# Kernel optimization log

Hardware: AMD Instinct MI355X
Metric: run time of the kernel (lower is better)

Reference implementation:

```python
import jax, jax.numpy as jnp
import numpy as np

B, V, C, G, D, H, W, N = 1, 4, 32, 8, 8, 240, 320, 9
EPS = 1e-5  # BatchNorm3d default eps


def grid_sample(img, grid, align_corners, zeros_pad):
    # img [B,C,Hs,Ws], grid [B,Hg,Wg,2] normalized coords; mirrors torch F.grid_sample bilinear
    Bi, Ci, Hs, Ws = img.shape
    gx, gy = grid[..., 0], grid[..., 1]
    if align_corners:
        ix = (gx + 1.0) * 0.5 * (Ws - 1)
        iy = (gy + 1.0) * 0.5 * (Hs - 1)
    else:
        ix = ((gx + 1.0) * Ws - 1.0) * 0.5
        iy = ((gy + 1.0) * Hs - 1.0) * 0.5
    x0 = jnp.floor(ix)
    y0 = jnp.floor(iy)
    wx1 = ix - x0
    wy1 = iy - y0

    def corner(xi, yi, wgt):
        xc = jnp.clip(xi, 0, Ws - 1).astype(jnp.int32)
        yc = jnp.clip(yi, 0, Hs - 1).astype(jnp.int32)
        v = jax.vmap(lambda im, yy, xx: im[:, yy, xx])(img, yc, xc)  # [B,C,Hg,Wg]
        if zeros_pad:
            valid = ((xi >= 0) & (xi <= Ws - 1) & (yi >= 0) & (yi <= Hs - 1)).astype(img.dtype)
            wgt = wgt * valid
        return v * wgt[:, None]

    return (corner(x0, y0, (1 - wx1) * (1 - wy1)) + corner(x0 + 1, y0, wx1 * (1 - wy1))
            + corner(x0, y0 + 1, (1 - wx1) * wy1) + corner(x0 + 1, y0 + 1, wx1 * wy1))


def differentiable_warping(src_fea, src_proj, ref_proj, depth):
    # src_fea [B,Cf,H,W], projs [B,4,4], depth [B,D,H,W] -> [B,Cf,D,H,W]
    Bi, Cf, Hs, Ws = src_fea.shape
    Dd = depth.shape[1]
    proj = src_proj @ jnp.linalg.inv(ref_proj)
    rot, trans = proj[:, :3, :3], proj[:, :3, 3:4]
    yy, xx = jnp.meshgrid(jnp.arange(Hs, dtype=jnp.float32), jnp.arange(Ws, dtype=jnp.float32), indexing='ij')
    xyz = jnp.stack([xx.ravel(), yy.ravel(), jnp.ones(Hs * Ws, jnp.float32)], axis=0)  # [3,HW]
    rot_xyz = jnp.einsum('bij,jk->bik', rot, xyz)  # [B,3,HW]
    pxyz = rot_xyz[:, :, None, :] * depth.reshape(Bi, 1, Dd, Hs * Ws) + trans[:, :, :, None]  # [B,3,D,HW]
    neg = pxyz[:, 2] <= 1e-3
    px = jnp.where(neg, float(Ws), pxyz[:, 0])
    py = jnp.where(neg, float(Hs), pxyz[:, 1])
    pz = jnp.where(neg, 1.0, pxyz[:, 2])
    gx = (px / pz) / ((Ws - 1) / 2.0) - 1.0
    gy = (py / pz) / ((Hs - 1) / 2.0) - 1.0
    grid = jnp.stack([gx, gy], axis=-1).reshape(Bi, Dd * Hs, Ws, 2)
    grid = jax.lax.stop_gradient(grid)  # torch builds the warp grid under no_grad
    warped = grid_sample(src_fea, grid, align_corners=True, zeros_pad=True)  # [B,Cf,D*H,W]
    return warped.reshape(Bi, Cf, Dd, Hs, Ws)


def conv_bn_relu(x, w, bn):
    # 1x1x1 Conv3d (no bias) + BatchNorm3d (inference) + ReLU; x [B,Ci,D,H,W]
    y = jnp.einsum('oi,bidhw->bodhw', w, x)
    g, b, m, v = bn
    s = g / jnp.sqrt(v + EPS)
    return jax.nn.relu(y * s[:, None, None, None] + (b - m * s)[:, None, None, None])


def conv1(x, w, b):
    return jnp.einsum('oi,bidhw->bodhw', w, x) + b[:, None, None, None]


def pixel_wise_net(sim, w0, bn0, w1, bn1, w2, b2):
    y = conv_bn_relu(sim, w0, bn0)
    y = conv_bn_relu(y, w1, bn1)
    y = jax.nn.sigmoid(conv1(y, w2, b2))[:, 0]  # [B,D,H,W]
    return jnp.max(y, axis=1, keepdims=True)  # [B,1,H,W]


def _forward(ref_feature, src_features, ref_proj, src_projs, depth_sample, grid, weight,
             pw_w0, pw_bn0, pw_w1, pw_bn1, pw_w2, pw_b2,
             sn_w0, sn_bn0, sn_w1, sn_bn1, sn_w2, sn_b2):
    Bi, Cf, Hs, Ws = ref_feature.shape
    Gq = pw_w0.shape[1]
    Dd = depth_sample.shape[1]
    ref_g = ref_feature.reshape(Bi, Gq, Cf // Gq, 1, Hs, Ws)
    sim_sum = jnp.zeros((Bi, Gq, Dd, Hs, Ws), jnp.float32)
    w_sum = jnp.zeros((Bi, 1, 1, Hs, Ws), jnp.float32)
    vws = []
    for v in range(src_features.shape[0]):  # small fixed view count
        warped = differentiable_warping(src_features[v], src_projs[v], ref_proj, depth_sample)
        warped = warped.reshape(Bi, Gq, Cf // Gq, Dd, Hs, Ws)
        sim = jnp.mean(warped * ref_g, axis=2)  # [B,G,D,H,W] group correlation
        vw = pixel_wise_net(sim, pw_w0, pw_bn0, pw_w1, pw_bn1, pw_w2, pw_b2)  # [B,1,H,W]
        vws.append(vw)
        sim_sum = sim_sum + sim * vw[:, :, None]
        w_sum = w_sum + vw[:, :, None]
    x = sim_sum / w_sum
    # SimilarityNet: conv stack -> neighbor grid_sample -> adaptive weighted sum
    y = conv_bn_relu(x, sn_w0, sn_bn0)
    y = conv_bn_relu(y, sn_w1, sn_bn1)
    y = conv1(y, sn_w2, sn_b2)[:, 0]  # [B,D,H,W]
    s = grid_sample(y, grid, align_corners=False, zeros_pad=False)  # border pad, [B,D,N*H,W]
    Nn = grid.shape[1] // Hs
    s = s.reshape(Bi, Dd, Nn, Hs, Ws)
    score_vol = jnp.sum(s * weight, axis=2)  # [B,D,H,W]
    score = jax.nn.softmax(score_vol, axis=1)  # exp(log_softmax) == softmax
    depth = jnp.sum(depth_sample * score, axis=1)  # [B,H,W] (is_inverse=False)
    view_weights = jax.lax.stop_gradient(jnp.concatenate(vws, axis=1))  # [B,V,H,W]
    return depth, score, view_weights


def setup_inputs():
    key = jax.random.key(0)
    ks = jax.random.split(key, 20)
    ref_feature = jax.random.normal(ks[0], (B, C, H, W), jnp.float32)
    src_features = jax.random.normal(ks[1], (V, B, C, H, W), jnp.float32)
    f = 500.0
    K = np.array([[f, 0, W / 2.0, 0], [0, f, H / 2.0, 0], [0, 0, 1, 0], [0, 0, 0, 1]], np.float32)
    ref_proj = jnp.asarray(np.tile(K[None], (B, 1, 1)))
    sp = []
    for tx, ty in [(20.0, 0.0), (-20.0, 0.0), (0.0, 10.0), (0.0, -10.0)]:
        E = np.eye(4, dtype=np.float32)
        E[0, 3], E[1, 3] = tx, ty
        sp.append(np.tile((K @ E)[None], (B, 1, 1)))
    src_projs = jnp.asarray(np.stack(sp))
    depth_sample = jnp.sort(425.0 + 510.0 * jax.random.uniform(ks[2], (B, D, H, W), jnp.float32), axis=1)
    # evaluation neighbor grid: per-pixel +-3px learned-style offsets, align_corners=False normalization
    dx = jax.random.uniform(ks[3], (B, N, H, W), minval=-3.0, maxval=3.0)
    dy = jax.random.uniform(ks[4], (B, N, H, W), minval=-3.0, maxval=3.0)
    xs = jnp.arange(W, dtype=jnp.float32)[None, None, None, :]
    ys = jnp.arange(H, dtype=jnp.float32)[None, None, :, None]
    gx = (2.0 * (xs + dx) + 1.0) / W - 1.0
    gy = (2.0 * (ys + dy) + 1.0) / H - 1.0
    grid = jnp.stack([gx, gy], -1).reshape(B, N * H, W, 2)
    weight = jax.random.uniform(ks[5], (B, D, N, H, W), jnp.float32)  # feature*depth weight in (0,1)

    def bn(k, c):
        k1, k2, k3, k4 = jax.random.split(k, 4)
        return jnp.stack([1.0 + 0.1 * jax.random.normal(k1, (c,)), 0.1 * jax.random.normal(k2, (c,)),
                          0.01 * jax.random.normal(k3, (c,)), 1.0 + 0.1 * jax.random.uniform(k4, (c,))])

    return dict(ref_feature=ref_feature, src_features=src_features, ref_proj=ref_proj,
                src_projs=src_projs, depth_sample=depth_sample, grid=grid, weight=weight,
                pw_w0=0.1 * jax.random.normal(ks[6], (16, G)), pw_bn0=bn(ks[7], 16),
                pw_w1=0.1 * jax.random.normal(ks[8], (8, 16)), pw_bn1=bn(ks[9], 8),
                pw_w2=0.1 * jax.random.normal(ks[10], (1, 8)), pw_b2=jnp.zeros((1,), jnp.float32),
                sn_w0=0.1 * jax.random.normal(ks[11], (16, G)), sn_bn0=bn(ks[12], 16),
                sn_w1=0.1 * jax.random.normal(ks[13], (8, 16)), sn_bn1=bn(ks[14], 8),
                sn_w2=0.1 * jax.random.normal(ks[15], (1, 8)), sn_b2=jnp.zeros((1,), jnp.float32))


def reference(ref_feature, src_features, ref_proj, src_projs, depth_sample, grid, weight,
              pw_w0, pw_bn0, pw_w1, pw_bn1, pw_w2, pw_b2,
              sn_w0, sn_bn0, sn_w1, sn_bn1, sn_w2, sn_b2):
    return _forward(ref_feature, src_features, ref_proj, src_projs, depth_sample, grid, weight,
                    pw_w0, pw_bn0, pw_w1, pw_bn1, pw_w2, pw_b2,
                    sn_w0, sn_bn0, sn_w1, sn_bn1, sn_w2, sn_b2)
```

## Files before the change

kernel.cpp:

```cpp
#include <hip/hip_runtime.h>
#include <hip/hip_fp16.h>
#include <cstdint>
#include <cstddef>

#define HH 240
#define WW 320
#define HWPIX 76800
#define NVIEW 4
#define NCH 32
#define NGRP 8
#define NDEP 8
#define NNEI 9
#define SPLANE (HWPIX * NCH)

#define OFF_PROJ 0
#define OFF_PW   48
#define OFF_SN   208
#define OFF_Y    640
#define OFF_SRCT 615040

typedef _Float16 h2 __attribute__((ext_vector_type(2)));

__device__ __forceinline__ float fdot2_(h2 a, h2 b, float c) {
#if __has_builtin(__builtin_amdgcn_fdot2)
  return __builtin_amdgcn_fdot2(a, b, c, false);
#else
  return c + (float)a.x * (float)b.x + (float)a.y * (float)b.y;
#endif
}
__device__ __forceinline__ h2 pk_(float a, float b) {
#if __has_builtin(__builtin_amdgcn_cvt_pkrtz)
  return __builtin_bit_cast(h2, __builtin_amdgcn_cvt_pkrtz(a, b));
#else
  h2 r; r.x = (_Float16)a; r.y = (_Float16)b; return r;
#endif
}

__device__ __forceinline__ float mlp_h(const float* __restrict__ p, const h2 x[4]) {
  const h2* w0 = (const h2*)p;
  const h2* w1 = (const h2*)(p + 64);
  const h2* w2 = (const h2*)(p + 128);
  h2 hx[8];
#pragma unroll
  for (int o = 0; o < 8; ++o) {
    float a0 = p[132 + 2 * o], a1 = p[132 + 2 * o + 1];
#pragma unroll
    for (int i = 0; i < 4; ++i) {
      a0 = fdot2_(w0[(2 * o) * 4 + i], x[i], a0);
      a1 = fdot2_(w0[(2 * o + 1) * 4 + i], x[i], a1);
    }
    hx[o] = pk_(fmaxf(a0, 0.0f), fmaxf(a1, 0.0f));
  }
  h2 hy[4];
#pragma unroll
  for (int o = 0; o < 4; ++o) {
    float a0 = p[148 + 2 * o], a1 = p[148 + 2 * o + 1];
#pragma unroll
    for (int i = 0; i < 8; ++i) {
      a0 = fdot2_(w1[(2 * o) * 8 + i], hx[i], a0);
      a1 = fdot2_(w1[(2 * o + 1) * 8 + i], hx[i], a1);
    }
    hy[o] = pk_(fmaxf(a0, 0.0f), fmaxf(a1, 0.0f));
  }
  float acc = p[156];
#pragma unroll
  for (int i = 0; i < 4; ++i) acc = fdot2_(w2[i], hy[i], acc);
  return acc;
}

__global__ void k_setup(const float* __restrict__ refP, const float* __restrict__ srcP,
                        const float* __restrict__ pw0, const float* __restrict__ pbn0,
                        const float* __restrict__ pw1, const float* __restrict__ pbn1,
                        const float* __restrict__ pw2, const float* __restrict__ pb2,
                        const float* __restrict__ sw0, const float* __restrict__ sbn0,
                        const float* __restrict__ sw1, const float* __restrict__ sbn1,
                        const float* __restrict__ sw2, const float* __restrict__ sb2,
                        float* __restrict__ ws) {
  int tid = threadIdx.x;
  if (tid == 578) {
    float a[4][8];
    for (int i = 0; i < 4; ++i)
      for (int j = 0; j < 4; ++j) { a[i][j] = refP[i * 4 + j]; a[i][4 + j] = (i == j) ? 1.0f : 0.0f; }
    for (int c = 0; c < 4; ++c) {
      int piv = c; float best = fabsf(a[c][c]);
      for (int r = c + 1; r < 4; ++r) { float t = fabsf(a[r][c]); if (t > best) { best = t; piv = r; } }
      if (piv != c) for (int j = 0; j < 8; ++j) { float t = a[c][j]; a[c][j] = a[piv][j]; a[piv][j] = t; }
      float inv = 1.0f / a[c][c];
      for (int j = 0; j < 8; ++j) a[c][j] *= inv;
      for (int r = 0; r < 4; ++r) if (r != c) {
        float f = a[r][c];
        for (int j = 0; j < 8; ++j) a[r][j] -= f * a[c][j];
      }
    }
    for (int v = 0; v < NVIEW; ++v) {
      const float* S = srcP + v * 16;
      for (int i = 0; i < 3; ++i)
        for (int j = 0; j < 4; ++j) {
          float p = S[i*4+0]*a[0][4+j] + S[i*4+1]*a[1][4+j] + S[i*4+2]*a[2][4+j] + S[i*4+3]*a[3][4+j];
          if (j < 3) ws[v * 12 + i * 3 + j] = p;
          else       ws[v * 12 + 9 + i] = p;
        }
    }
    return;
  }
  if (tid >= 578) return;
  int k = tid / 289;
  int j = tid - k * 289;
  const float* W0 = k ? sw0 : pw0;  const float* B0 = k ? sbn0 : pbn0;
  const float* W1 = k ? sw1 : pw1;  const float* B1 = k ? sbn1 : pbn1;
  const float* W2 = k ? sw2 : pw2;  const float* B2 = k ? sb2 : pb2;
  float* p = ws + (k ? OFF_SN : OFF_PW);
  __half* w0h = (__half*)p;
  __half* w1h = (__half*)(p + 64);
  __half* w2h = (__half*)(p + 128);
  if (j < 128) {
    int o = j >> 3;
    float s = B0[o] / sqrtf(B0[48 + o] + 1e-5f);
    w0h[j] = __float2half_rn(W0[j] * s * 0.25f);
  } else if (j < 256) {
    int idx = j - 128; int o = idx >> 4;
    float s = B1[o] / sqrtf(B1[24 + o] + 1e-5f);
    w1h[idx] = __float2half_rn(W1[idx] * s);
  } else if (j < 264) {
    w2h[j - 256] = __float2half_rn(W2[j - 256]);
  } else if (j < 280) {
    int o = j - 264;
    float s = B0[o] / sqrtf(B0[48 + o] + 1e-5f);
    p[132 + o] = B0[16 + o] - B0[32 + o] * s;
  } else if (j < 288) {
    int o = j - 280;
    float s = B1[o] / sqrtf(B1[24 + o] + 1e-5f);
    p[148 + o] = B1[8 + o] - B1[16 + o] * s;
  } else {
    p[156] = B2[0];
  }
}

__global__ __launch_bounds__(256) void k_transpose(const float* __restrict__ src,
                                                   const float* __restrict__ ref,
                                                   __half* __restrict__ dst, int total) {
  int t = blockIdx.x * 256 + threadIdx.x;
  if (t >= total) return;
  int c8 = t & 3;
  int vp = t >> 2;
  int v = vp / HWPIX;
  int pix = vp - v * HWPIX;
  const float* s = (v < NVIEW) ? (src + ((size_t)(v * NCH + c8 * 8)) * HWPIX + pix)
                               : (ref + ((size_t)(c8 * 8)) * HWPIX + pix);
  union { h2 h[4]; float4 f; } u;
  u.h[0] = pk_(s[0],         s[HWPIX]);
  u.h[1] = pk_(s[2 * HWPIX], s[3 * HWPIX]);
  u.h[2] = pk_(s[4 * HWPIX], s[5 * HWPIX]);
  u.h[3] = pk_(s[6 * HWPIX], s[7 * HWPIX]);
  reinterpret_cast<float4*>(dst + (size_t)vp * NCH)[c8] = u.f;
}

__device__ __forceinline__ void tap_f16(const __half* __restrict__ p, float wtf,
                                        h2 wp[16], bool first) {
  _Float16 wh = (_Float16)wtf;
  h2 wt2 = h2{wh, wh};
  const float4* q = reinterpret_cast<const float4*>(p);
#pragma unroll
  for (int i = 0; i < 4; ++i) {
    union { float4 f; h2 h[4]; } u; u.f = q[i];
#pragma unroll
    for (int c = 0; c < 4; ++c) {
      if (first) wp[4 * i + c] = u.h[c] * wt2;
      else       wp[4 * i + c] += u.h[c] * wt2;
    }
  }
}

template <int MODE>
__global__ __launch_bounds__(256) void k_main(
    const float* __restrict__ ref, const float* __restrict__ src,
    const __half* __restrict__ srcT,
    const float* __restrict__ depthS, const float* __restrict__ wsc,
    float* __restrict__ ybuf, float* __restrict__ outVW) {
  int t = blockIdx.x * 256 + threadIdx.x;
  int d = t & 7;
  int pix = t >> 3;
  int h = pix / WW;
  int w = pix - h * WW;
  float fx = (float)w, fy = (float)h;

  h2 rc[16];
  float rcf[(MODE == 0) ? NCH : 1];
  if (MODE == 1) {
    const float4* rp = reinterpret_cast<const float4*>(srcT + (size_t)NVIEW * SPLANE + (size_t)pix * NCH);
#pragma unroll
    for (int i = 0; i < 4; ++i) {
      union { float4 f; h2 h[4]; } u; u.f = rp[i];
      rc[4*i] = u.h[0]; rc[4*i+1] = u.h[1]; rc[4*i+2] = u.h[2]; rc[4*i+3] = u.h[3];
    }
  } else {
#pragma unroll
    for (int c = 0; c < NCH; ++c) rcf[c] = ref[c * HWPIX + pix];
  }
  float dep = depthS[d * HWPIX + pix];

  float ssum[NGRP];
#pragma unroll
  for (int g = 0; g < NGRP; ++g) ssum[g] = 0.0f;
  float wsum = 0.0f;

#pragma unroll 1
  for (int v = 0; v < NVIEW; ++v) {
    const float* pr = wsc + v * 12;
    float rx = fmaf(pr[0], fx, fmaf(pr[1], fy, pr[2]));
    float ry = fmaf(pr[3], fx, fmaf(pr[4], fy, pr[5]));
    float rz = fmaf(pr[6], fx, fmaf(pr[7], fy, pr[8]));
    float pz_ = fmaf(rz, dep, pr[11]);
    bool neg = (pz_ <= 0.001f);
    float px_ = neg ? (float)WW : fmaf(rx, dep, pr[9]);
    float py_ = neg ? (float)HH : fmaf(ry, dep, pr[10]);
    float rpz = neg ? 1.0f : __fdividef(1.0f, pz_);
    float ix = px_ * rpz;
    float iy = py_ * rpz;
    float x0f = floorf(ix), y0f = floorf(iy);
    float wx1 = ix - x0f, wy1 = iy - y0f;
    float wx0 = 1.0f - wx1, wy0 = 1.0f - wy1;
    float x1f = x0f + 1.0f, y1f = y0f + 1.0f;
    float vx0 = (x0f >= 0.0f && x0f <= (float)(WW - 1)) ? 1.0f : 0.0f;
    float vx1 = (x1f >= 0.0f && x1f <= (float)(WW - 1)) ? 1.0f : 0.0f;
    float vy0 = (y0f >= 0.0f && y0f <= (float)(HH - 1)) ? 1.0f : 0.0f;
    float vy1 = (y1f >= 0.0f && y1f <= (float)(HH - 1)) ? 1.0f : 0.0f;
    int xa = (int)fminf(fmaxf(x0f, 0.0f), (float)(WW - 1));
    int xb = (int)fminf(fmaxf(x1f, 0.0f), (float)(WW - 1));
    int ya = (int)fminf(fmaxf(y0f, 0.0f), (float)(HH - 1));
    int yb = (int)fminf(fmaxf(y1f, 0.0f), (float)(HH - 1));
    float w00 = wx0 * wy0 * vx0 * vy0;
    float w01 = wx1 * wy0 * vx1 * vy0;
    float w10 = wx0 * wy1 * vx0 * vy1;
    float w11 = wx1 * wy1 * vx1 * vy1;

    float simf[NGRP];
    if (MODE == 1) {
      const __half* vbase = srcT + (size_t)v * SPLANE;
      h2 wp[16];
      tap_f16(vbase + (size_t)(ya * WW + xa) * NCH, w00, wp, true);
      tap_f16(vbase + (size_t)(ya * WW + xb) * NCH, w01, wp, false);
      tap_f16(vbase + (size_t)(yb * WW + xa) * NCH, w10, wp, false);
      tap_f16(vbase + (size_t)(yb * WW + xb) * NCH, w11, wp, false);
#pragma unroll
      for (int g = 0; g < NGRP; ++g)
        simf[g] = fdot2_(wp[2*g+1], rc[2*g+1], fdot2_(wp[2*g], rc[2*g], 0.0f));
    } else {
      const float* base = src + (size_t)v * NCH * HWPIX;
      const float* p00 = base + ya * WW + xa;
      const float* p01 = base + ya * WW + xb;
      const float* p10 = base + yb * WW + xa;
      const float* p11 = base + yb * WW + xb;
#pragma unroll
      for (int g = 0; g < NGRP; ++g) {
        float acc = 0.0f;
#pragma unroll
        for (int cc = 0; cc < 4; ++cc) {
          size_t o = (size_t)(g * 4 + cc) * HWPIX;
          float wv = w00 * p00[o] + w01 * p01[o] + w10 * p10[o] + w11 * p11[o];
          acc = fmaf(wv, rcf[g * 4 + cc], acc);
        }
        simf[g] = acc;
      }
    }

    h2 x[4];
#pragma unroll
    for (int i = 0; i < 4; ++i) x[i] = pk_(simf[2*i], simf[2*i+1]);
    float sc = mlp_h(wsc + OFF_PW, x);
    sc = fmaxf(sc, __shfl_xor(sc, 1, 8));
    sc = fmaxf(sc, __shfl_xor(sc, 2, 8));
    sc = fmaxf(sc, __shfl_xor(sc, 4, 8));
    float vw = __fdividef(1.0f, 1.0f + __expf(-sc));
#pragma unroll
    for (int g = 0; g < NGRP; ++g) ssum[g] = fmaf(simf[g], vw, ssum[g]);
    wsum += vw;
    if (d == 0) outVW[v * HWPIX + pix] = vw;
  }

  float rw = __fdividef(1.0f, wsum);
  h2 xg[4];
#pragma unroll
  for (int i = 0; i < 4; ++i) xg[i] = pk_(ssum[2*i] * rw, ssum[2*i+1] * rw);
  float yv = mlp_h(wsc + OFF_SN, xg);
  ybuf[pix * NDEP + d] = yv;
}

__global__ __launch_bounds__(256) void k_score(
    const float* __restrict__ grid, const float* __restrict__ weight,
    const float* __restrict__ depthS, const float* __restrict__ ybuf,
    float* __restrict__ out) {
  int t = blockIdx.x * 256 + threadIdx.x;
  int d = t & 7;
  int pix = t >> 3;
  int h = pix / WW;
  int w = pix - h * WW;
  float sv = 0.0f;
#pragma unroll 1
  for (int n = 0; n < NNEI; ++n) {
    int gi = ((n * HH + h) * WW + w) * 2;
    float gx = grid[gi], gy = grid[gi + 1];
    float ix = ((gx + 1.0f) * (float)WW - 1.0f) * 0.5f;
    float iy = ((gy + 1.0f) * (float)HH - 1.0f) * 0.5f;
    float x0f = floorf(ix), y0f = floorf(iy);
    float wx1 = ix - x0f, wy1 = iy - y0f;
    float wx0 = 1.0f - wx1, wy0 = 1.0f - wy1;
    int xa = (int)fminf(fmaxf(x0f, 0.0f), (float)(WW - 1));
    int xb = (int)fminf(fmaxf(x0f + 1.0f, 0.0f), (float)(WW - 1));
    int ya = (int)fminf(fmaxf(y0f, 0.0f), (float)(HH - 1));
    int yb2 = (int)fminf(fmaxf(y0f + 1.0f, 0.0f), (float)(HH - 1));
    float v00 = ybuf[(ya * WW + xa) * NDEP + d], v01 = ybuf[(ya * WW + xb) * NDEP + d];
    float v10 = ybuf[(yb2 * WW + xa) * NDEP + d], v11 = ybuf[(yb2 * WW + xb) * NDEP + d];
    float s = wy0 * fmaf(wx0, v00, wx1 * v01) + wy1 * fmaf(wx0, v10, wx1 * v11);
    float wn = weight[((d * NNEI + n) * HH + h) * WW + w];
    sv = fmaf(s, wn, sv);
  }
  float m = sv;
  m = fmaxf(m, __shfl_xor(m, 1, 8));
  m = fmaxf(m, __shfl_xor(m, 2, 8));
  m = fmaxf(m, __shfl_xor(m, 4, 8));
  float e = __expf(sv - m);
  float s8 = e;
  s8 += __shfl_xor(s8, 1, 8);
  s8 += __shfl_xor(s8, 2, 8);
  s8 += __shfl_xor(s8, 4, 8);
  float sc = __fdividef(e, s8);
  out[HWPIX + d * HWPIX + pix] = sc;
  float dp = depthS[d * HWPIX + pix] * sc;
  dp += __shfl_xor(dp, 1, 8);
  dp += __shfl_xor(dp, 2, 8);
  dp += __shfl_xor(dp, 4, 8);
  if (d == 0) out[pix] = dp;
}

extern "C" void kernel_launch(void* const* d_in, const int* in_sizes, int n_in,
                              void* d_out, int out_size, void* d_ws, size_t ws_size,
                              hipStream_t stream) {
  const float* ref    = (const float*)d_in[0];
  const float* src    = (const float*)d_in[1];
  const float* refP   = (const float*)d_in[2];
  const float* srcP   = (const float*)d_in[3];
  const float* depthS = (const float*)d_in[4];
  const float* grid   = (const float*)d_in[5];
  const float* weight = (const float*)d_in[6];
  float* out = (float*)d_out;
  float* ws  = (float*)d_ws;
  __half* srcT = (__half*)(ws + OFF_SRCT);

  size_t need = (size_t)OFF_SRCT * 4 + (size_t)5 * SPLANE * 2;
  int mode = (ws_size >= need) ? 1 : 0;

  k_setup<<<1, 640, 0, stream>>>(refP, srcP,
                                 (const float*)d_in[7], (const float*)d_in[8],
                                 (const float*)d_in[9], (const float*)d_in[10],
                                 (const float*)d_in[11], (const float*)d_in[12],
                                 (const float*)d_in[13], (const float*)d_in[14],
                                 (const float*)d_in[15], (const float*)d_in[16],
                                 (const float*)d_in[17], (const float*)d_in[18], ws);
  if (mode == 1) {
    int total = 5 * HWPIX * 4;
    k_transpose<<<(total + 255) / 256, 256, 0, stream>>>(src, ref, srcT, total);
    k_main<1><<<(HWPIX * 8) / 256, 256, 0, stream>>>(ref, src, srcT, depthS, ws,
                                                     ws + OFF_Y, out + 9 * HWPIX);
  } else {
    k_main<0><<<(HWPIX * 8) / 256, 256, 0, stream>>>(ref, src, srcT, depthS, ws,
                                                     ws + OFF_Y, out + 9 * HWPIX);
  }
  k_score<<<(HWPIX * 8) / 256, 256, 0, stream>>>(grid, weight, depthS, ws + OFF_Y, out);
}
```

Measured before the change: 91.60 us.

## Process all depths per thread in score kernel, transpose depth, use DPP max

Restructures k_score so each thread handles one pixel and all 8 depths. It loads the 8 depth values of each bilinear corner as two float4 reads and does softmax and the depth expectation in registers instead of with cross-lane shuffles. The transpose kernel also writes a pixel-major copy of the depth samples, which k_main and k_score read with coalesced or vector loads. The 8-lane max reduction in k_main is replaced by DPP moves instead of shuffles. The risk is that k_score now runs 8x fewer threads, so it has less parallelism to hide latency, and its weight reads stride across depth planes per thread.

New measurement: 93.31 us. About the same (+1.9%).

```diff
diff --git a/kernel.cpp b/kernel.cpp
--- a/kernel.cpp
+++ b/kernel.cpp
@@ -18,6 +18,7 @@
 #define OFF_SN   208
 #define OFF_Y    640
 #define OFF_SRCT 615040
+#define OFF_DEPT (OFF_SRCT + 5 * SPLANE / 2)
 
 typedef _Float16 h2 __attribute__((ext_vector_type(2)));
 
@@ -34,6 +35,20 @@
 #else
   h2 r; r.x = (_Float16)a; r.y = (_Float16)b; return r;
 #endif
+}
+
+__device__ __forceinline__ float maxd8(float x) {
+  int xi = __builtin_bit_cast(int, x);
+  int t = __builtin_amdgcn_mov_dpp(xi, 0xB1, 0xF, 0xF, true);
+  x = fmaxf(x, __builtin_bit_cast(float, t));
+  xi = __builtin_bit_cast(int, x);
+  t = __builtin_amdgcn_mov_dpp(xi, 0x4E, 0xF, 0xF, true);
+  x = fmaxf(x, __builtin_bit_cast(float, t));
+  xi = __builtin_bit_cast(int, x);
+  int a = __builtin_amdgcn_update_dpp(xi, xi, 0x124, 0xF, 0x5, false);
+  int b = __builtin_amdgcn_update_dpp(a,  xi, 0x12C, 0xF, 0xA, false);
+  x = fmaxf(x, __builtin_bit_cast(float, b));
+  return x;
 }
 
 __device__ __forceinline__ float mlp_h(const float* __restrict__ p, const h2 x[4]) {
@@ -138,9 +153,23 @@
 
 __global__ __launch_bounds__(256) void k_transpose(const float* __restrict__ src,
                                                    const float* __restrict__ ref,
-                                                   __half* __restrict__ dst, int total) {
+                                                   const float* __restrict__ depthS,
+                                                   __half* __restrict__ dst,
+                                                   float* __restrict__ dep_t, int total) {
   int t = blockIdx.x * 256 + threadIdx.x;
   if (t >= total) return;
+  const int base = 5 * HWPIX * 4;
+  if (t >= base) {
+    int pix = t - base;
+    float4 a, b;
+    a.x = depthS[0 * HWPIX + pix]; a.y = depthS[1 * HWPIX + pix];
+    a.z = depthS[2 * HWPIX + pix]; a.w = depthS[3 * HWPIX + pix];
+    b.x = depthS[4 * HWPIX + pix]; b.y = depthS[5 * HWPIX + pix];
+    b.z = depthS[6 * HWPIX + pix]; b.w = depthS[7 * HWPIX + pix];
+    float4* o = reinterpret_cast<float4*>(dep_t + (size_t)pix * NDEP);
+    o[0] = a; o[1] = b;
+    return;
+  }
   int c8 = t & 3;
   int vp = t >> 2;
   int v = vp / HWPIX;
@@ -175,7 +204,8 @@
 __global__ __launch_bounds__(256) void k_main(
     const float* __restrict__ ref, const float* __restrict__ src,
     const __half* __restrict__ srcT,
-    const float* __restrict__ depthS, const float* __restrict__ wsc,
+    const float* __restrict__ depthS, const float* __restrict__ dep_t,
+    const float* __restrict__ wsc,
     float* __restrict__ ybuf, float* __restrict__ outVW) {
   int t = blockIdx.x * 256 + threadIdx.x;
   int d = t & 7;
@@ -197,7 +227,7 @@
 #pragma unroll
     for (int c = 0; c < NCH; ++c) rcf[c] = ref[c * HWPIX + pix];
   }
-  float dep = depthS[d * HWPIX + pix];
+  float dep = (MODE == 1) ? dep_t[(size_t)pix * NDEP + d] : depthS[d * HWPIX + pix];
 
   float ssum[NGRP];
 #pragma unroll
@@ -268,9 +298,7 @@
 #pragma unroll
     for (int i = 0; i < 4; ++i) x[i] = pk_(simf[2*i], simf[2*i+1]);
     float sc = mlp_h(wsc + OFF_PW, x);
-    sc = fmaxf(sc, __shfl_xor(sc, 1, 8));
-    sc = fmaxf(sc, __shfl_xor(sc, 2, 8));
-    sc = fmaxf(sc, __shfl_xor(sc, 4, 8));
+    sc = maxd8(sc);
     float vw = __fdividef(1.0f, 1.0f + __expf(-sc));
 #pragma unroll
     for (int g = 0; g < NGRP; ++g) ssum[g] = fmaf(simf[g], vw, ssum[g]);
@@ -288,14 +316,15 @@
 
 __global__ __launch_bounds__(256) void k_score(
     const float* __restrict__ grid, const float* __restrict__ weight,
-    const float* __restrict__ depthS, const float* __restrict__ ybuf,
-    float* __restrict__ out) {
-  int t = blockIdx.x * 256 + threadIdx.x;
-  int d = t & 7;
-  int pix = t >> 3;
+    const float* __restrict__ depthS, const float* __restrict__ dep_t,
+    const float* __restrict__ ybuf, float* __restrict__ out, int useDT) {
+  int pix = blockIdx.x * 256 + threadIdx.x;
   int h = pix / WW;
   int w = pix - h * WW;
-  float sv = 0.0f;
+  float sv[NDEP];
+#pragma unroll
+  for (int d = 0; d < NDEP; ++d) sv[d] = 0.0f;
+
 #pragma unroll 1
   for (int n = 0; n < NNEI; ++n) {
     int gi = ((n * HH + h) * WW + w) * 2;
@@ -309,28 +338,58 @@
     int xb = (int)fminf(fmaxf(x0f + 1.0f, 0.0f), (float)(WW - 1));
     int ya = (int)fminf(fmaxf(y0f, 0.0f), (float)(HH - 1));
     int yb2 = (int)fminf(fmaxf(y0f + 1.0f, 0.0f), (float)(HH - 1));
-    float v00 = ybuf[(ya * WW + xa) * NDEP + d], v01 = ybuf[(ya * WW + xb) * NDEP + d];
-    float v10 = ybuf[(yb2 * WW + xa) * NDEP + d], v11 = ybuf[(yb2 * WW + xb) * NDEP + d];
-    float s = wy0 * fmaf(wx0, v00, wx1 * v01) + wy1 * fmaf(wx0, v10, wx1 * v11);
-    float wn = weight[((d * NNEI + n) * HH + h) * WW + w];
-    sv = fmaf(s, wn, sv);
-  }
-  float m = sv;
-  m = fmaxf(m, __shfl_xor(m, 1, 8));
-  m = fmaxf(m, __shfl_xor(m, 2, 8));
-  m = fmaxf(m, __shfl_xor(m, 4, 8));
-  float e = __expf(sv - m);
-  float s8 = e;
-  s8 += __shfl_xor(s8, 1, 8);
-  s8 += __shfl_xor(s8, 2, 8);
-  s8 += __shfl_xor(s8, 4, 8);
-  float sc = __fdividef(e, s8);
-  out[HWPIX + d * HWPIX + pix] = sc;
-  float dp = depthS[d * HWPIX + pix] * sc;
-  dp += __shfl_xor(dp, 1, 8);
-  dp += __shfl_xor(dp, 2, 8);
-  dp += __shfl_xor(dp, 4, 8);
-  if (d == 0) out[pix] = dp;
+    const float4* p00 = reinterpret_cast<const float4*>(ybuf + (size_t)(ya * WW + xa) * NDEP);
+    const float4* p01 = reinterpret_cast<const float4*>(ybuf + (size_t)(ya * WW + xb) * NDEP);
+    const float4* p10 = reinterpret_cast<const float4*>(ybuf + (size_t)(yb2 * WW + xa) * NDEP);
+    const float4* p11 = reinterpret_cast<const float4*>(ybuf + (size_t)(yb2 * WW + xb) * NDEP);
+    float4 a00 = p00[0], b00 = p00[1];
+    float4 a01 = p01[0], b01 = p01[1];
+    float4 a10 = p10[0], b10 = p10[1];
+    float4 a11 = p11[0], b11 = p11[1];
+    const float* v00 = (const float*)&a00;
+    const float* v01 = (const float*)&a01;
+    const float* v10 = (const float*)&a10;
+    const float* v11 = (const float*)&a11;
+    const float* u00 = (const float*)&b00;
+    const float* u01 = (const float*)&b01;
+    const float* u10 = (const float*)&b10;
+    const float* u11 = (const float*)&b11;
+#pragma unroll
+    for (int d = 0; d < NDEP; ++d) {
+      float c00 = (d < 4) ? v00[d] : u00[d - 4];
+      float c01 = (d < 4) ? v01[d] : u01[d - 4];
+      float c10 = (d < 4) ? v10[d] : u10[d - 4];
+      float c11 = (d < 4) ? v11[d] : u11[d - 4];
+      float s = wy0 * fmaf(wx0, c00, wx1 * c01) + wy1 * fmaf(wx0, c10, wx1 * c11);
+      float wn = weight[((size_t)(d * NNEI + n) * HH + h) * WW + w];
+      sv[d] = fmaf(s, wn, sv[d]);
+    }
+  }
+  float m = sv[0];
+#pragma unroll
+  for (int d = 1; d < NDEP; ++d) m = fmaxf(m, sv[d]);
+  float e[NDEP], s8 = 0.0f;
+#pragma unroll
+  for (int d = 0; d < NDEP; ++d) { e[d] = __expf(sv[d] - m); s8 += e[d]; }
+  float r = __fdividef(1.0f, s8);
+  float dpv[NDEP];
+  if (useDT) {
+    const float4* dp4 = reinterpret_cast<const float4*>(dep_t + (size_t)pix * NDEP);
+    float4 da = dp4[0], db = dp4[1];
+    dpv[0]=da.x; dpv[1]=da.y; dpv[2]=da.z; dpv[3]=da.w;
+    dpv[4]=db.x; dpv[5]=db.y; dpv[6]=db.z; dpv[7]=db.w;
+  } else {
+#pragma unroll
+    for (int d = 0; d < NDEP; ++d) dpv[d] = depthS[d * HWPIX + pix];
+  }
+  float dp = 0.0f;
+#pragma unroll
+  for (int d = 0; d < NDEP; ++d) {
+    float sc = e[d] * r;
+    out[HWPIX + d * HWPIX + pix] = sc;
+    dp = fmaf(dpv[d], sc, dp);
+  }
+  out[pix] = dp;
 }
 
 extern "C" void kernel_launch(void* const* d_in, const int* in_sizes, int n_in,
@@ -346,8 +405,9 @@
   float* out = (float*)d_out;
   float* ws  = (float*)d_ws;
   __half* srcT = (__half*)(ws + OFF_SRCT);
-
-  size_t need = (size_t)OFF_SRCT * 4 + (size_t)5 * SPLANE * 2;
+  float* dep_t = ws + OFF_DEPT;
+
+  size_t need = ((size_t)OFF_DEPT + (size_t)NDEP * HWPIX) * 4;
   int mode = (ws_size >= need) ? 1 : 0;
 
   k_setup<<<1, 640, 0, stream>>>(refP, srcP,
@@ -358,13 +418,13 @@
                                  (const float*)d_in[15], (const float*)d_in[16],
                                  (const float*)d_in[17], (const float*)d_in[18], ws);
   if (mode == 1) {
-    int total = 5 * HWPIX * 4;
-    k_transpose<<<(total + 255) / 256, 256, 0, stream>>>(src, ref, srcT, total);
-    k_main<1><<<(HWPIX * 8) / 256, 256, 0, stream>>>(ref, src, srcT, depthS, ws,
+    int total = 5 * HWPIX * 4 + HWPIX;
+    k_transpose<<<(total + 255) / 256, 256, 0, stream>>>(src, ref, depthS, srcT, dep_t, total);
+    k_main<1><<<(HWPIX * 8) / 256, 256, 0, stream>>>(ref, src, srcT, depthS, dep_t, ws,
                                                      ws + OFF_Y, out + 9 * HWPIX);
   } else {
-    k_main<0><<<(HWPIX * 8) / 256, 256, 0, stream>>>(ref, src, srcT, depthS, ws,
+    k_main<0><<<(HWPIX * 8) / 256, 256, 0, stream>>>(ref, src, srcT, depthS, dep_t, ws,
                                                      ws + OFF_Y, out + 9 * HWPIX);
   }
-  k_score<<<(HWPIX * 8) / 256, 256, 0, stream>>>(grid, weight, depthS, ws + OFF_Y, out);
-}
+  k_score<<<HWPIX / 256, 256, 0, stream>>>(grid, weight, depthS, dep_t, ws + OFF_Y, out, mode);
+}
```
